# Kernel tuning notes

Measured on AMD Instinct MI355X. Metric: run time of the kernel, lower is better.

Reference implementation:

```python
import jax, jax.numpy as jnp
import numpy as np

B, L_SEQ, D, P, N_LAYERS, V = 2, 4096, 128, 64, 2, 32000
EPS_LN = 1e-5
EPS_Z = 1e-8


def _layernorm(x, g, b):
    mu = jnp.mean(x, axis=-1, keepdims=True)
    var = jnp.mean(jnp.square(x - mu), axis=-1, keepdims=True)
    return (x - mu) * jax.lax.rsqrt(var + EPS_LN) * g + b


def setup_inputs() -> dict:
    key = jax.random.key(0)
    ks = jax.random.split(key, 16)
    tokens = jax.random.randint(ks[0], (B, L_SEQ), 0, V)
    s = 0.02
    embed = jax.random.normal(ks[1], (V, D), jnp.float32) * s
    pos_emb = jax.random.normal(ks[2], (L_SEQ, D), jnp.float32) * s
    Wq = jax.random.normal(ks[3], (N_LAYERS, D, D), jnp.float32) * s
    Wk = jax.random.normal(ks[4], (N_LAYERS, D, D), jnp.float32) * s
    Wv = jax.random.normal(ks[5], (N_LAYERS, D, D), jnp.float32) * s
    # orthonormal random projection per layer (QR, like torch.linalg.qr reduced)
    rng = np.random.default_rng(0)
    proj_np = np.stack([np.linalg.qr(rng.standard_normal((D, P)))[0] for _ in range(N_LAYERS)])
    proj = jnp.asarray(proj_np, jnp.float32)
    ln_g = jnp.ones((N_LAYERS, D), jnp.float32)
    ln_b = jnp.zeros((N_LAYERS, D), jnp.float32)
    W1 = jax.random.normal(ks[6], (N_LAYERS, D, 4 * D), jnp.float32) * s
    b1 = jnp.zeros((N_LAYERS, 4 * D), jnp.float32)
    W2 = jax.random.normal(ks[7], (N_LAYERS, 4 * D, D), jnp.float32) * s
    b2 = jnp.zeros((N_LAYERS, D), jnp.float32)
    Wout = jax.random.normal(ks[8], (D, V), jnp.float32) * s
    return {"tokens": tokens, "embed": embed, "pos_emb": pos_emb, "Wq": Wq, "Wk": Wk,
            "Wv": Wv, "proj": proj, "ln_g": ln_g, "ln_b": ln_b, "W1": W1, "b1": b1,
            "W2": W2, "b2": b2, "Wout": Wout}


def reference(tokens, embed, pos_emb, Wq, Wk, Wv, proj, ln_g, ln_b, W1, b1, W2, b2, Wout):
    # h: [B, L, D]
    h = embed[tokens] + pos_emb[None, :, :]
    for i in range(N_LAYERS):
        residual = h
        # linear (FAVOR-style) attention, single head
        q = h @ Wq[i]
        k = h @ Wk[i]
        v = h @ Wv[i]
        q_prime = jax.nn.elu(q @ proj[i]) + 1.0  # [B, L, P]
        k_prime = jax.nn.elu(k @ proj[i]) + 1.0
        kv = jnp.einsum('blp,bld->bpd', k_prime, v)      # [B, P, D]
        num = jnp.einsum('blp,bpd->bld', q_prime, kv)     # [B, L, D]
        z = 1.0 / (jnp.sum(q_prime, axis=-1, keepdims=True) + EPS_Z)
        attn = num * z
        # LayerNorm then FFN (dropout = identity, eval mode)
        a = _layernorm(attn, ln_g[i], ln_b[i])
        f = jax.nn.gelu(a @ W1[i] + b1[i], approximate=False) @ W2[i] + b2[i]
        h = residual + f
    logits = h @ Wout  # [B, L, V]
    return logits
```

## Files before the change

kernel.cpp:

```cpp
#include <hip/hip_runtime.h>
#include <hip/hip_bf16.h>

#define BATCH 2
#define LSEQ 4096
#define M (BATCH*LSEQ)
#define D 128
#define P 64
#define NL 2
#define VOCAB 32000
#define DFF 512

typedef __attribute__((ext_vector_type(8))) short bf16x8_t;
typedef __attribute__((ext_vector_type(4))) float f32x4_t;

__device__ inline unsigned short f2bf(float f) {
    unsigned int u = __float_as_uint(f);
    unsigned int r = (u + 0x7fffu + ((u >> 16) & 1u)) >> 16;
    return (unsigned short)r;
}
__device__ inline float bf2f(unsigned short u) {
    return __uint_as_float(((unsigned int)u) << 16);
}

__global__ __launch_bounds__(256) void k_prep_all(const int* __restrict__ tokens,
                                                  const float* __restrict__ embed,
                                                  const float* __restrict__ pos,
                                                  float* __restrict__ h,
                                                  unsigned short* __restrict__ hb,
                                                  const float* __restrict__ Wout,
                                                  unsigned short* __restrict__ WT,
                                                  const float* __restrict__ Wq,
                                                  const float* __restrict__ Wk,
                                                  const float* __restrict__ Wv,
                                                  const float* __restrict__ proj,
                                                  unsigned short* __restrict__ bqkv,
                                                  const float* __restrict__ W1,
                                                  unsigned short* __restrict__ W1T,
                                                  const float* __restrict__ W2,
                                                  unsigned short* __restrict__ W2T) {
    __shared__ float tile[32][33];
    int b = blockIdx.x;
    int tid = threadIdx.x;
    if (b < 1024) {
        int gid = b * 256 + tid;
        int row = gid >> 5;
        int d4  = gid & 31;
        int l = row & (LSEQ - 1);
        int tok = tokens[row];
        float4 a = ((const float4*)(embed + (size_t)tok * D))[d4];
        float4 p4 = ((const float4*)(pos + (size_t)l * D))[d4];
        a.x += p4.x; a.y += p4.y; a.z += p4.z; a.w += p4.w;
        ((float4*)(h + (size_t)row * D))[d4] = a;
        ushort4 u; u.x = f2bf(a.x); u.y = f2bf(a.y); u.z = f2bf(a.z); u.w = f2bf(a.w);
        ((ushort4*)(hb + (size_t)row * D))[d4] = u;
    } else if (b < 5024) {
        int bb = b - 1024;
        int v0 = (bb % 1000) * 32, d0 = (bb / 1000) * 32;
        int tx = tid & 31, ty = tid >> 5;
        for (int i = ty; i < 32; i += 8)
            tile[i][tx] = Wout[(size_t)(d0 + i) * VOCAB + v0 + tx];
        __syncthreads();
        for (int i = ty; i < 32; i += 8)
            WT[(size_t)(v0 + i) * D + d0 + tx] = f2bf(tile[tx][i]);
    } else if (b < 5280) {
        int idx = (b - 5024) * 256 + tid;
        int d = idx & 127;
        int r = (idx >> 7) & 255;
        int l = idx >> 15;
        const float* WqL = Wq + (size_t)l * D * D;
        const float* WkL = Wk + (size_t)l * D * D;
        const float* WvL = Wv + (size_t)l * D * D;
        const float* pjL = proj + (size_t)l * D * P;
        float val;
        if (r < 128) {
            const float* W = (r < 64) ? WqL : WkL;
            int p = r & 63;
            float s = 0.f;
            for (int e = 0; e < D; e++) s = fmaf(W[d * D + e], pjL[e * P + p], s);
            val = s;
        } else {
            val = WvL[d * D + (r - 128)];
        }
        bqkv[((size_t)l * 256 + r) * D + d] = f2bf(val);
    } else if (b < 5792) {
        int idx = (b - 5280) * 256 + tid;
        int d = idx & 127;
        int n = (idx >> 7) & 511;
        int l = idx >> 16;
        W1T[((size_t)l * DFF + n) * D + d] = f2bf(W1[((size_t)l * D + d) * DFF + n]);
    } else {
        int idx = (b - 5792) * 256 + tid;
        int f = idx & 511;
        int n = (idx >> 9) & 127;
        int l = idx >> 16;
        W2T[((size_t)l * D + n) * DFF + f] = f2bf(W2[((size_t)l * DFF + f) * D + n]);
    }
}

__global__ __launch_bounds__(256) void k_qkvp(const unsigned short* __restrict__ hb,
                                              const unsigned short* __restrict__ Bt,
                                              float* __restrict__ qp, float* __restrict__ kp,
                                              unsigned short* __restrict__ vb,
                                              float* __restrict__ kv) {
    if (blockIdx.x == 0) {
        float4 z = make_float4(0.f, 0.f, 0.f, 0.f);
        float4* kv4 = (float4*)kv;
        for (int i = threadIdx.x; i < BATCH * P * D / 4; i += 256) kv4[i] = z;
    }
    int r0 = blockIdx.x * 32;
    int wid = threadIdx.x >> 6;
    int lane = threadIdx.x & 63;
    int c0 = wid * 64;
    int lr = lane & 15;
    int lk = (lane >> 4) * 8;
    const short* Ap = (const short*)hb;
    const short* Bp = (const short*)Bt;
    f32x4_t acc[2][4] = {};
    #pragma unroll
    for (int kc = 0; kc < 4; kc++) {
        bf16x8_t af[2], bfr[4];
        #pragma unroll
        for (int mi = 0; mi < 2; mi++)
            af[mi] = *(const bf16x8_t*)(Ap + (size_t)(r0 + mi * 16 + lr) * D + kc * 32 + lk);
        #pragma unroll
        for (int ni = 0; ni < 4; ni++)
            bfr[ni] = *(const bf16x8_t*)(Bp + (size_t)(c0 + ni * 16 + lr) * D + kc * 32 + lk);
        #pragma unroll
        for (int mi = 0; mi < 2; mi++)
            #pragma unroll
            for (int ni = 0; ni < 4; ni++)
                acc[mi][ni] = __builtin_amdgcn_mfma_f32_16x16x32_bf16(af[mi], bfr[ni], acc[mi][ni], 0, 0, 0);
    }
    int orow = (lane >> 4) * 4;
    if (wid < 2) {
        float* out = (wid == 0) ? qp : kp;
        #pragma unroll
        for (int mi = 0; mi < 2; mi++)
            #pragma unroll
            for (int ni = 0; ni < 4; ni++)
                #pragma unroll
                for (int j = 0; j < 4; j++) {
                    float x = acc[mi][ni][j];
                    float e = x > 0.f ? x + 1.f : __expf(x);
                    out[(size_t)(r0 + mi * 16 + orow + j) * P + ni * 16 + lr] = e;
                }
    } else {
        int cb = (wid - 2) * 64;
        #pragma unroll
        for (int mi = 0; mi < 2; mi++)
            #pragma unroll
            for (int ni = 0; ni < 4; ni++)
                #pragma unroll
                for (int j = 0; j < 4; j++)
                    vb[(size_t)(r0 + mi * 16 + orow + j) * D + cb + ni * 16 + lr] = f2bf(acc[mi][ni][j]);
    }
}

__global__ void k_kvpart(const float* __restrict__ kp, const unsigned short* __restrict__ vb,
                         float* __restrict__ kv) {
    int p = blockIdx.x, ch = blockIdx.y, b = blockIdx.z, d = threadIdx.x;
    const float* kpb = kp + (size_t)b * LSEQ * P + p;
    const unsigned short* vbp = vb + (size_t)b * LSEQ * D + d;
    int l0 = ch * 256;
    float a0 = 0.f, a1 = 0.f, a2 = 0.f, a3 = 0.f;
    for (int l = l0; l < l0 + 256; l += 4) {
        a0 = fmaf(kpb[(size_t)l * P],       bf2f(vbp[(size_t)l * D]),       a0);
        a1 = fmaf(kpb[(size_t)(l + 1) * P], bf2f(vbp[(size_t)(l + 1) * D]), a1);
        a2 = fmaf(kpb[(size_t)(l + 2) * P], bf2f(vbp[(size_t)(l + 2) * D]), a2);
        a3 = fmaf(kpb[(size_t)(l + 3) * P], bf2f(vbp[(size_t)(l + 3) * D]), a3);
    }
    atomicAdd(&kv[((size_t)b * P + p) * D + d], (a0 + a1) + (a2 + a3));
}

#define TSTRIDE 520
#define ABSTRIDE 136
__global__ __launch_bounds__(256) void k_attnffn(const float* __restrict__ qp,
                                                 const float* __restrict__ kv,
                                                 const float* __restrict__ lng,
                                                 const float* __restrict__ lnb,
                                                 const unsigned short* __restrict__ W1T,
                                                 const float* __restrict__ b1,
                                                 const unsigned short* __restrict__ W2T,
                                                 const float* __restrict__ b2,
                                                 float* __restrict__ h,
                                                 unsigned short* __restrict__ hb) {
    __shared__ unsigned short abt[16 * ABSTRIDE];
    __shared__ unsigned short tl[16 * TSTRIDE];
    int r0 = blockIdx.x * 16;
    int b = r0 >> 12;
    int tid = threadIdx.x;
    {
        int row16 = tid >> 4;
        int dq = tid & 15;
        int d0 = dq * 8;
        const float* qpr = qp + (size_t)(r0 + row16) * P;
        const float4* kv4 = (const float4*)(kv + (size_t)b * P * D);
        float num[8] = {};
        float zs = 0.f;
        #pragma unroll 8
        for (int p = 0; p < P; p++) {
            float qv = qpr[p];
            zs += qv;
            float4 v0 = kv4[p * 32 + dq * 2];
            float4 v1 = kv4[p * 32 + dq * 2 + 1];
            num[0] = fmaf(qv, v0.x, num[0]);
            num[1] = fmaf(qv, v0.y, num[1]);
            num[2] = fmaf(qv, v0.z, num[2]);
            num[3] = fmaf(qv, v0.w, num[3]);
            num[4] = fmaf(qv, v1.x, num[4]);
            num[5] = fmaf(qv, v1.y, num[5]);
            num[6] = fmaf(qv, v1.z, num[6]);
            num[7] = fmaf(qv, v1.w, num[7]);
        }
        float rz = 1.f / (zs + 1e-8f);
        float attn[8];
        float s = 0.f;
        #pragma unroll
        for (int j = 0; j < 8; j++) { attn[j] = num[j] * rz; s += attn[j]; }
        #pragma unroll
        for (int m = 1; m < 16; m <<= 1) s += __shfl_xor(s, m);
        float mu = s * (1.f / 128.f);
        float dv[8];
        float s2 = 0.f;
        #pragma unroll
        for (int j = 0; j < 8; j++) { dv[j] = attn[j] - mu; s2 = fmaf(dv[j], dv[j], s2); }
        #pragma unroll
        for (int m = 1; m < 16; m <<= 1) s2 += __shfl_xor(s2, m);
        float rs = rsqrtf(s2 * (1.f / 128.f) + 1e-5f);
        #pragma unroll
        for (int j = 0; j < 8; j++) {
            float o = dv[j] * rs * lng[d0 + j] + lnb[d0 + j];
            abt[row16 * ABSTRIDE + d0 + j] = f2bf(o);
        }
    }
    __syncthreads();
    int wid = tid >> 6;
    int lane = tid & 63;
    int lr = lane & 15;
    int lk = (lane >> 4) * 8;
    int orow = (lane >> 4) * 4;
    const short* B1 = (const short*)W1T;
    int c0 = wid * 128;
    f32x4_t acc1[8] = {};
    #pragma unroll
    for (int kc = 0; kc < 4; kc++) {
        bf16x8_t af = *(const bf16x8_t*)(abt + lr * ABSTRIDE + kc * 32 + lk);
        bf16x8_t bfr[8];
        #pragma unroll
        for (int ni = 0; ni < 8; ni++)
            bfr[ni] = *(const bf16x8_t*)(B1 + (size_t)(c0 + ni * 16 + lr) * D + kc * 32 + lk);
        #pragma unroll
        for (int ni = 0; ni < 8; ni++)
            acc1[ni] = __builtin_amdgcn_mfma_f32_16x16x32_bf16(af, bfr[ni], acc1[ni], 0, 0, 0);
    }
    #pragma unroll
    for (int ni = 0; ni < 8; ni++) {
        int col = c0 + ni * 16 + lr;
        float bias = b1[col];
        #pragma unroll
        for (int j = 0; j < 4; j++) {
            float x = acc1[ni][j] + bias;
            float g = 0.5f * x * (1.f + erff(x * 0.70710678f));
            tl[(orow + j) * TSTRIDE + col] = f2bf(g);
        }
    }
    __syncthreads();
    int c2 = wid * 32;
    const short* B2 = (const short*)W2T;
    f32x4_t acc2[2] = {};
    #pragma unroll 4
    for (int kc = 0; kc < 16; kc++) {
        bf16x8_t af, bfr[2];
        af = *(const bf16x8_t*)(tl + (size_t)lr * TSTRIDE + kc * 32 + lk);
        #pragma unroll
        for (int ni = 0; ni < 2; ni++)
            bfr[ni] = *(const bf16x8_t*)(B2 + (size_t)(c2 + ni * 16 + lr) * DFF + kc * 32 + lk);
        #pragma unroll
        for (int ni = 0; ni < 2; ni++)
            acc2[ni] = __builtin_amdgcn_mfma_f32_16x16x32_bf16(af, bfr[ni], acc2[ni], 0, 0, 0);
    }
    #pragma unroll
    for (int ni = 0; ni < 2; ni++) {
        int col = c2 + ni * 16 + lr;
        float bias = b2[col];
        #pragma unroll
        for (int j = 0; j < 4; j++) {
            size_t idx = (size_t)(r0 + orow + j) * D + col;
            float hn = h[idx] + acc2[ni][j] + bias;
            h[idx] = hn;
            hb[idx] = f2bf(hn);
        }
    }
}

__global__ __launch_bounds__(256) void k_gemm_out(const unsigned short* __restrict__ A,
                                                  const unsigned short* __restrict__ Bt,
                                                  float* __restrict__ C) {
    __shared__ unsigned short bl[128 * 128];
    int bx = blockIdx.x;
    int bg = blockIdx.y;
    int tid = threadIdx.x;
    {
        const bf16x8_t* src = (const bf16x8_t*)((const short*)Bt + (size_t)bx * 128 * D);
        int row = tid >> 1;
        int base = (tid & 1) * 128;
        char* dst = (char*)bl + row * 256;
        #pragma unroll
        for (int i = 0; i < 8; i++) {
            int boff = base + i * 16;
            *(bf16x8_t*)(dst + (boff ^ ((row & 7) << 4))) = src[tid * 8 + i];
        }
    }
    __syncthreads();
    int wid = tid >> 6;
    int lane = tid & 63;
    int wr = wid >> 1, wc = wid & 1;
    int lr = lane & 15;
    int hi = lane >> 4;
    int lk = hi * 8;
    int col0 = bx * 128 + wc * 64;
    const short* Ap = (const short*)A;
    #pragma unroll 1
    for (int w = 0; w < 4; w++) {
        int row0 = (bg * 4 + w) * 128 + wr * 64;
        f32x4_t acc[4][4] = {};
        #pragma unroll
        for (int kc = 0; kc < 4; kc++) {
            bf16x8_t af[4], bfr[4];
            #pragma unroll
            for (int mi = 0; mi < 4; mi++)
                af[mi] = *(const bf16x8_t*)(Ap + (size_t)(row0 + mi * 16 + lr) * D + kc * 32 + lk);
            #pragma unroll
            for (int ni = 0; ni < 4; ni++) {
                int brow = wc * 64 + ni * 16 + lr;
                int boff = kc * 64 + hi * 16;
                bfr[ni] = *(const bf16x8_t*)((const char*)bl + brow * 256 + (boff ^ ((brow & 7) << 4)));
            }
            #pragma unroll
            for (int mi = 0; mi < 4; mi++)
                #pragma unroll
                for (int ni = 0; ni < 4; ni++)
                    acc[mi][ni] = __builtin_amdgcn_mfma_f32_16x16x32_bf16(af[mi], bfr[ni], acc[mi][ni], 0, 0, 0);
        }
        int orow = hi * 4;
        #pragma unroll
        for (int mi = 0; mi < 4; mi++)
            #pragma unroll
            for (int j = 0; j < 4; j++)
                #pragma unroll
                for (int ni = 0; ni < 4; ni++)
                    __builtin_nontemporal_store(acc[mi][ni][j],
                        &C[(size_t)(row0 + mi * 16 + orow + j) * VOCAB + col0 + ni * 16 + lr]);
    }
}

extern "C" void kernel_launch(void* const* d_in, const int* in_sizes, int n_in,
                              void* d_out, int out_size, void* d_ws, size_t ws_size,
                              hipStream_t stream) {
    const int*   tokens = (const int*)d_in[0];
    const float* embed  = (const float*)d_in[1];
    const float* pos    = (const float*)d_in[2];
    const float* Wq     = (const float*)d_in[3];
    const float* Wk     = (const float*)d_in[4];
    const float* Wv     = (const float*)d_in[5];
    const float* proj   = (const float*)d_in[6];
    const float* lng    = (const float*)d_in[7];
    const float* lnb    = (const float*)d_in[8];
    const float* W1     = (const float*)d_in[9];
    const float* b1     = (const float*)d_in[10];
    const float* W2     = (const float*)d_in[11];
    const float* b2     = (const float*)d_in[12];
    const float* Wout   = (const float*)d_in[13];
    float* out = (float*)d_out;
    char* ws = (char*)d_ws;

    float*          h    = (float*)(ws);
    unsigned short* hb   = (unsigned short*)(ws + ((size_t)4  << 20));
    float*          qp   = (float*)(ws + ((size_t)6  << 20));
    float*          kp   = (float*)(ws + ((size_t)8  << 20));
    unsigned short* vb   = (unsigned short*)(ws + ((size_t)10 << 20));
    float*          kv   = (float*)(ws + ((size_t)13 << 20));
    unsigned short* wt   = (unsigned short*)(ws + ((size_t)24 << 20));
    unsigned short* bqkv = (unsigned short*)(ws + ((size_t)32 << 20));
    unsigned short* w1t  = (unsigned short*)(ws + ((size_t)33 << 20));
    unsigned short* w2t  = (unsigned short*)(ws + ((size_t)34 << 20));

    k_prep_all<<<dim3(6304), dim3(256), 0, stream>>>(tokens, embed, pos, h, hb,
                                                     Wout, wt, Wq, Wk, Wv, proj, bqkv,
                                                     W1, w1t, W2, w2t);

    for (int i = 0; i < NL; i++) {
        k_qkvp<<<dim3(M / 32), dim3(256), 0, stream>>>(hb, bqkv + (size_t)i * 256 * D, qp, kp, vb, kv);
        k_kvpart<<<dim3(P, 16, BATCH), dim3(128), 0, stream>>>(kp, vb, kv);
        k_attnffn<<<dim3(M / 16), dim3(256), 0, stream>>>(qp, kv, lng + (size_t)i * D, lnb + (size_t)i * D,
                                                          w1t + (size_t)i * DFF * D, b1 + (size_t)i * DFF,
                                                          w2t + (size_t)i * D * DFF, b2 + (size_t)i * D, h, hb);
    }

    k_gemm_out<<<dim3(VOCAB / 128, M / 128 / 4), dim3(256), 0, stream>>>(hb, wt, out);
}
```

Before: 365.7 us.

## Stage output GEMM tiles through LDS for coalesced 16-byte logits stores

The output GEMM now gives each wave a 32x128 tile instead of a 64x64 one, which changes the MFMA fragment layout. The accumulators are staged through a per-wave padded LDS buffer, so each lane can issue 16-byte nontemporal stores that cover full 512-byte row segments. This targets the scattered 4-byte stores into the large logits matrix, which is likely a major share of kernel time. The cost is extra LDS traffic, LDS capacity use, and explicit waits. The ordering relies on wave-local synchronisation without barriers.

```diff
diff --git a/kernel.cpp b/kernel.cpp
--- a/kernel.cpp
+++ b/kernel.cpp
@@ -297,6 +297,7 @@
                                                   const unsigned short* __restrict__ Bt,
                                                   float* __restrict__ C) {
     __shared__ unsigned short bl[128 * 128];
+    __shared__ float cl[4][8 * 132];
     int bx = blockIdx.x;
     int bg = blockIdx.y;
     int tid = threadIdx.x;
@@ -314,43 +315,57 @@
     __syncthreads();
     int wid = tid >> 6;
     int lane = tid & 63;
-    int wr = wid >> 1, wc = wid & 1;
     int lr = lane & 15;
     int hi = lane >> 4;
     int lk = hi * 8;
-    int col0 = bx * 128 + wc * 64;
+    float* clw = cl[wid];
     const short* Ap = (const short*)A;
     #pragma unroll 1
     for (int w = 0; w < 4; w++) {
-        int row0 = (bg * 4 + w) * 128 + wr * 64;
-        f32x4_t acc[4][4] = {};
+        int row0 = (bg * 4 + w) * 128 + wid * 32;
+        f32x4_t acc[2][8] = {};
         #pragma unroll
         for (int kc = 0; kc < 4; kc++) {
-            bf16x8_t af[4], bfr[4];
-            #pragma unroll
-            for (int mi = 0; mi < 4; mi++)
+            bf16x8_t af[2], bfr[8];
+            #pragma unroll
+            for (int mi = 0; mi < 2; mi++)
                 af[mi] = *(const bf16x8_t*)(Ap + (size_t)(row0 + mi * 16 + lr) * D + kc * 32 + lk);
             #pragma unroll
-            for (int ni = 0; ni < 4; ni++) {
-                int brow = wc * 64 + ni * 16 + lr;
+            for (int ni = 0; ni < 8; ni++) {
+                int brow = ni * 16 + lr;
                 int boff = kc * 64 + hi * 16;
                 bfr[ni] = *(const bf16x8_t*)((const char*)bl + brow * 256 + (boff ^ ((brow & 7) << 4)));
             }
             #pragma unroll
-            for (int mi = 0; mi < 4; mi++)
+            for (int mi = 0; mi < 2; mi++)
                 #pragma unroll
-                for (int ni = 0; ni < 4; ni++)
+                for (int ni = 0; ni < 8; ni++)
                     acc[mi][ni] = __builtin_amdgcn_mfma_f32_16x16x32_bf16(af[mi], bfr[ni], acc[mi][ni], 0, 0, 0);
         }
-        int orow = hi * 4;
-        #pragma unroll
-        for (int mi = 0; mi < 4; mi++)
-            #pragma unroll
-            for (int j = 0; j < 4; j++)
+        #pragma unroll
+        for (int c = 0; c < 4; c++) {
+            int mi = c >> 1;
+            int hp = c & 1;
+            if ((hi >> 1) == hp) {
+                int rbase = (hi & 1) * 4;
                 #pragma unroll
-                for (int ni = 0; ni < 4; ni++)
-                    __builtin_nontemporal_store(acc[mi][ni][j],
-                        &C[(size_t)(row0 + mi * 16 + orow + j) * VOCAB + col0 + ni * 16 + lr]);
+                for (int ni = 0; ni < 8; ni++)
+                    #pragma unroll
+                    for (int j = 0; j < 4; j++)
+                        clw[(rbase + j) * 132 + ni * 16 + lr] = acc[mi][ni][j];
+            }
+            asm volatile("s_waitcnt lgkmcnt(0)" ::: "memory");
+            float* Cb = C + (size_t)(row0 + mi * 16 + hp * 8) * VOCAB + bx * 128;
+            #pragma unroll
+            for (int k = 0; k < 4; k++) {
+                int idx = k * 64 + lane;
+                int rr = idx >> 5;
+                int c4 = idx & 31;
+                f32x4_t v = *(const f32x4_t*)(clw + rr * 132 + c4 * 4);
+                __builtin_nontemporal_store(v, (f32x4_t*)(Cb + (size_t)rr * VOCAB + c4 * 4));
+            }
+            asm volatile("" ::: "memory");
+        }
     }
 }
 
```

After: 329.3 us. 9.9% less time.
